# Kernel tuning notes

Hardware: AMD Instinct MI355X
Metric: run time of the kernel (lower is better)

Reference implementation:

```python
import jax, jax.numpy as jnp
import numpy as np

N = 50000      # nodes
E = 800000     # edges
IN = 128       # in_channels
H = 256        # hidden_channels
EMB = 128      # embedding_size
R = 4          # num_relations
HEADS = 2


def setup_inputs() -> dict:
    key = jax.random.key(0)
    ks = jax.random.split(key, 20)
    w = lambda k, shape: jax.random.normal(k, shape, dtype=jnp.float32) * 0.05
    return dict(
        x=jax.random.normal(ks[0], (N, IN), dtype=jnp.float32),
        edge_index=jax.random.randint(ks[1], (2, E), 0, N, dtype=jnp.int32),
        edge_type=jax.random.randint(ks[2], (E,), 0, R, dtype=jnp.int32),
        sage1_Wl=w(ks[3], (IN, H)), sage1_Wr=w(ks[4], (IN, H)), sage1_b=jnp.zeros((H,), jnp.float32),
        sage2_Wl=w(ks[5], (H, H)), sage2_Wr=w(ks[6], (H, H)), sage2_b=jnp.zeros((H,), jnp.float32),
        gat_W=w(ks[7], (H, HEADS * H)), gat_att_src=w(ks[8], (HEADS, H)), gat_att_dst=w(ks[9], (HEADS, H)),
        gat_b=jnp.zeros((H,), jnp.float32),
        rgcn_Wrel=w(ks[10], (R, H, EMB)), rgcn_Wroot=w(ks[11], (H, EMB)), rgcn_b=jnp.zeros((EMB,), jnp.float32),
        fusion_W=w(ks[12], (H + H + EMB, EMB)), fusion_b=jnp.zeros((EMB,), jnp.float32),
    )


def _segmean(msg, seg, num_segments):
    s = jax.ops.segment_sum(msg, seg, num_segments=num_segments)
    c = jax.ops.segment_sum(jnp.ones((seg.shape[0], 1), msg.dtype), seg, num_segments=num_segments)
    return s / jnp.maximum(c, 1.0)


def _sage(x, src, dst, Wl, Wr, b, n):
    # SAGEConv: lin_l(mean_j x_j) + lin_r(x_i)
    agg = _segmean(x[src], dst, n)
    return agg @ Wl + x @ Wr + b


def _gat(x, src, dst, W, a_src, a_dst, b, n):
    # GATConv heads=2, concat=False (head average), add_self_loops=True
    loop = jnp.arange(n, dtype=src.dtype)
    src = jnp.concatenate([src, loop])
    dst = jnp.concatenate([dst, loop])
    h = (x @ W).reshape(n, HEADS, -1)                 # [N, heads, H]
    al_src = (h * a_src).sum(-1)                      # [N, heads]
    al_dst = (h * a_dst).sum(-1)                      # [N, heads]
    e = jax.nn.leaky_relu(al_src[src] + al_dst[dst], 0.2)   # [E', heads]
    m = jax.ops.segment_max(e, dst, num_segments=n)          # stable softmax per dst node
    ex = jnp.exp(e - m[dst])
    den = jax.ops.segment_sum(ex, dst, num_segments=n)
    alpha = ex / jnp.maximum(den[dst], 1e-16)
    out = jax.ops.segment_sum(alpha[:, :, None] * h[src], dst, num_segments=n)  # [N, heads, H]
    return out.mean(axis=1) + b


def _rgcn(x, src, dst, etype, Wrel, Wroot, b, n, r):
    # RGCNConv: sum_r mean_{j in N_r(i)} W_r x_j + W_root x_i + b
    xt = jnp.einsum('nh,rhe->rne', x, Wrel)           # [R, N, EMB]
    m = xt[etype, src]                                # [E, EMB]
    seg = dst * r + etype                             # per (node, relation) segment
    agg = _segmean(m, seg, n * r).reshape(n, r, -1).sum(axis=1)
    return agg + x @ Wroot + b


def reference(x, edge_index, edge_type,
              sage1_Wl, sage1_Wr, sage1_b,
              sage2_Wl, sage2_Wr, sage2_b,
              gat_W, gat_att_src, gat_att_dst, gat_b,
              rgcn_Wrel, rgcn_Wroot, rgcn_b,
              fusion_W, fusion_b):
    src, dst = edge_index[0], edge_index[1]
    n = x.shape[0]
    x1 = jax.nn.relu(_sage(x, src, dst, sage1_Wl, sage1_Wr, sage1_b, n))
    # dropout(p=0.2) is identity in eval mode
    x_sage = jax.nn.relu(_sage(x1, src, dst, sage2_Wl, sage2_Wr, sage2_b, n))
    x_gat = jax.nn.relu(_gat(x_sage, src, dst, gat_W, gat_att_src, gat_att_dst, gat_b, n))
    x_rgcn = _rgcn(x_gat, src, dst, edge_type, rgcn_Wrel, rgcn_Wroot, rgcn_b, n, R)
    x_all = jnp.concatenate([x_sage, x_gat, x_rgcn], axis=1)
    out = x_all @ fusion_W + fusion_b
    norm = jnp.maximum(jnp.linalg.norm(out, axis=1, keepdims=True), 1e-12)
    return out / norm
```

## Files before the change

### kernel.cpp

```cpp
#include <hip/hip_runtime.h>
#include <math.h>

constexpr int NN   = 50000;
constexpr int NE   = 800000;
constexpr int NREL = 4;
constexpr int NB   = (NN + 255) / 256;

typedef __attribute__((ext_vector_type(8))) short bfrag;
typedef __attribute__((ext_vector_type(4))) float floatx4;

__device__ inline unsigned short bf16_rne(float x) {
  unsigned u = __float_as_uint(x);
  unsigned r = (u + 0x7FFFu + ((u >> 16) & 1u)) >> 16;
  return (unsigned short)r;
}
__device__ inline float bf2f(unsigned short h) {
  return __uint_as_float((unsigned)h << 16);
}
__device__ inline void split2(float x, unsigned short& h, unsigned short& l) {
  h = bf16_rne(x);
  l = bf16_rne(x - bf2f(h));
}

__global__ void k_counts(const int* __restrict__ src, const int* __restrict__ dst,
                         const int* __restrict__ et, int* deg, int* cntrel) {
  int e = blockIdx.x * blockDim.x + threadIdx.x;
  if (e < NE) {
    int d = dst[e];
    atomicAdd(&deg[d], 1);
    atomicAdd(&cntrel[d * NREL + et[e]], 1);
  }
}

__global__ void k_scan1(const int* __restrict__ deg, int* bsum) {
  __shared__ int sm[256];
  int i = blockIdx.x * 256 + threadIdx.x;
  sm[threadIdx.x] = (i < NN) ? deg[i] : 0;
  __syncthreads();
  for (int s = 128; s; s >>= 1) {
    if (threadIdx.x < s) sm[threadIdx.x] += sm[threadIdx.x + s];
    __syncthreads();
  }
  if (threadIdx.x == 0) bsum[blockIdx.x] = sm[0];
}
__global__ void k_scan2(const int* __restrict__ bsum, int* boff, int* rowptr) {
  if (threadIdx.x == 0 && blockIdx.x == 0) {
    int acc = 0;
    for (int b = 0; b < NB; ++b) { boff[b] = acc; acc += bsum[b]; }
    rowptr[NN] = NE;
  }
}
__global__ void k_scan3(const int* __restrict__ deg, const int* __restrict__ boff,
                        int* rowptr) {
  __shared__ int sm[256];
  int i = blockIdx.x * 256 + threadIdx.x;
  int v = (i < NN) ? deg[i] : 0;
  sm[threadIdx.x] = v;
  __syncthreads();
  for (int s = 1; s < 256; s <<= 1) {
    int t = (threadIdx.x >= s) ? sm[threadIdx.x - s] : 0;
    __syncthreads();
    sm[threadIdx.x] += t;
    __syncthreads();
  }
  if (i < NN) rowptr[i] = boff[blockIdx.x] + sm[threadIdx.x] - v;
}

__global__ void k_fill(const int* __restrict__ src, const int* __restrict__ dst,
                       const int* __restrict__ et, const int* __restrict__ rowptr,
                       int* cursor, int* srcs, int* ets) {
  int e = blockIdx.x * blockDim.x + threadIdx.x;
  if (e >= NE) return;
  int d = dst[e];
  int pos = rowptr[d] + atomicAdd(&cursor[d], 1);
  srcs[pos] = src[e];
  ets[pos]  = et[e];
}

#define PK_N 14
__device__ __constant__ const int PK_BASE[PK_N]  = {0,1,2,3,4,4,5,5,5,5,6,7,7,7};
__device__ __constant__ const int PK_EOFF[PK_N]  = {0,0,0,0,0,256,0,32768,65536,98304,0,0,32768,65536};
__device__ __constant__ const int PK_K[PK_N]     = {128,128,256,256,256,256,256,256,256,256,256,256,256,128};
__device__ __constant__ const int PK_LDB[PK_N]   = {256,256,256,256,512,512,128,128,128,128,128,128,128,128};
__device__ __constant__ const int PK_START[PK_N] = {0,4096,8192,16384,24576,32768,40960,45056,49152,53248,57344,61440,65536,69632};
constexpr int PK_TOTAL = 71680;
constexpr int BF_S1WL = 0,     BF_S1WR = 4096,  BF_S2WL = 8192,  BF_S2WR = 16384;
constexpr int BF_GATW0 = 24576, BF_GATW1 = 32768, BF_WREL = 40960, BF_WROOT = 57344;
constexpr int BF_FW0 = 61440,  BF_FW1 = 65536,  BF_FW2 = 69632;

__global__ void k_pack(const float* b0, const float* b1, const float* b2, const float* b3,
                       const float* b4, const float* b5, const float* b6, const float* b7,
                       unsigned short* __restrict__ Bh) {
  int f = blockIdx.x * 256 + threadIdx.x;
  if (f >= PK_TOTAL) return;
  int m = 0;
#pragma unroll
  for (int i = 1; i < PK_N; ++i) if (f >= PK_START[i]) m = i;
  const float* bases[8] = {b0,b1,b2,b3,b4,b5,b6,b7};
  int lf = f - PK_START[m];
  int K = PK_K[m], ldb = PK_LDB[m];
  int Kq16 = K << 1;
  int ntile = lf / Kq16;
  int rem = lf - ntile * Kq16;
  int kq = rem >> 4, c = rem & 15;
  const float* sp = bases[PK_BASE[m]] + PK_EOFF[m] + (size_t)(kq * 8) * ldb + ntile * 16 + c;
#pragma unroll
  for (int j = 0; j < 8; ++j)
    Bh[(size_t)f * 8 + j] = bf16_rne(sp[(size_t)j * ldb]);
}

__global__ void k_split(const float* __restrict__ x, unsigned short* __restrict__ xh,
                        unsigned short* __restrict__ xl, long total4) {
  long i = (long)blockIdx.x * blockDim.x + threadIdx.x;
  if (i >= total4) return;
  float4 v = ((const float4*)x)[i];
  ushort4 h, l;
  split2(v.x, h.x, l.x); split2(v.y, h.y, l.y);
  split2(v.z, h.z, l.z); split2(v.w, h.w, l.w);
  ((ushort4*)xh)[i] = h;
  ((ushort4*)xl)[i] = l;
}

__global__ void k_mean128p(const unsigned short* __restrict__ ih, const int* __restrict__ rowptr,
                           const int* __restrict__ srcs,
                           unsigned short* __restrict__ oh, unsigned short* __restrict__ ol) {
  int node = blockIdx.x * 4 + (threadIdx.x >> 6);
  int lane = threadIdx.x & 63;
  if (node >= NN) return;
  int p0 = rowptr[node], p1 = rowptr[node + 1];
  float2 acc = make_float2(0.f, 0.f);
  int p = p0;
  for (; p + 4 <= p1; p += 4) {
    int s0 = srcs[p], s1 = srcs[p+1], s2 = srcs[p+2], s3 = srcs[p+3];
    ushort2 v0 = ((const ushort2*)(ih + ((size_t)s0 << 7)))[lane];
    ushort2 v1 = ((const ushort2*)(ih + ((size_t)s1 << 7)))[lane];
    ushort2 v2 = ((const ushort2*)(ih + ((size_t)s2 << 7)))[lane];
    ushort2 v3 = ((const ushort2*)(ih + ((size_t)s3 << 7)))[lane];
    acc.x += (bf2f(v0.x) + bf2f(v1.x)) + (bf2f(v2.x) + bf2f(v3.x));
    acc.y += (bf2f(v0.y) + bf2f(v1.y)) + (bf2f(v2.y) + bf2f(v3.y));
  }
  for (; p < p1; ++p) {
    int s = srcs[p];
    ushort2 hv = ((const ushort2*)(ih + ((size_t)s << 7)))[lane];
    acc.x += bf2f(hv.x); acc.y += bf2f(hv.y);
  }
  float inv = (p1 > p0) ? 1.0f / (float)(p1 - p0) : 0.0f;
  ushort2 h, l;
  split2(acc.x * inv, h.x, l.x); split2(acc.y * inv, h.y, l.y);
  size_t o = ((size_t)node << 7) + lane * 2;
  *(ushort2*)(oh + o) = h;
  *(ushort2*)(ol + o) = l;
}

__global__ void k_mean256p(const unsigned short* __restrict__ ih, const int* __restrict__ rowptr,
                           const int* __restrict__ srcs,
                           unsigned short* __restrict__ oh, unsigned short* __restrict__ ol) {
  int node = blockIdx.x * 4 + (threadIdx.x >> 6);
  int lane = threadIdx.x & 63;
  if (node >= NN) return;
  int p0 = rowptr[node], p1 = rowptr[node + 1];
  float4 acc = make_float4(0.f, 0.f, 0.f, 0.f);
  int p = p0;
  for (; p + 8 <= p1; p += 8) {
    int ss[8]; ushort4 xr[8];
#pragma unroll
    for (int j = 0; j < 8; ++j) ss[j] = srcs[p + j];
#pragma unroll
    for (int j = 0; j < 8; ++j)
      xr[j] = *(const ushort4*)(ih + ((size_t)ss[j] << 8) + lane * 4);
#pragma unroll
    for (int j = 0; j < 8; ++j) {
      acc.x += bf2f(xr[j].x); acc.y += bf2f(xr[j].y);
      acc.z += bf2f(xr[j].z); acc.w += bf2f(xr[j].w);
    }
  }
  for (; p < p1; ++p) {
    int s = srcs[p];
    ushort4 hv = *(const ushort4*)(ih + ((size_t)s << 8) + lane * 4);
    acc.x += bf2f(hv.x); acc.y += bf2f(hv.y);
    acc.z += bf2f(hv.z); acc.w += bf2f(hv.w);
  }
  float inv = (p1 > p0) ? 1.0f / (float)(p1 - p0) : 0.0f;
  ushort4 h, l;
  split2(acc.x * inv, h.x, l.x); split2(acc.y * inv, h.y, l.y);
  split2(acc.z * inv, h.z, l.z); split2(acc.w * inv, h.w, l.w);
  size_t o = ((size_t)node << 8) + lane * 4;
  *(ushort4*)(oh + o) = h;
  *(ushort4*)(ol + o) = l;
}

__global__ __launch_bounds__(256)
void k_gemm_mfma(const unsigned short* __restrict__ Bph,
                 const unsigned short* A0h, const unsigned short* A0l, int lda0, int bf0, int K0,
                 const unsigned short* A1h, const unsigned short* A1l, int lda1, int bf1, int K1,
                 const unsigned short* A2h, const unsigned short* A2l, int lda2, int bf2, int K2,
                 const float* __restrict__ bias, float* Cf,
                 unsigned short* Ch, unsigned short* Cl,
                 int M, int Nc, float scale, int do_relu, int zsB, long zsC, int xtmode)
{
  __shared__ short Ash[8*64*8], Asl[8*64*8], Bsh[8*64*8];
  const int tid  = threadIdx.x;
  const int lane = tid & 63;
  const int wv   = tid >> 6;
  const int wm   = wv >> 1, wn = wv & 1;
  const int nwg = gridDim.x * gridDim.y;
  const int d   = blockIdx.x + gridDim.x * blockIdx.y;
  const int q   = nwg >> 3, r = nwg & 7;
  const int xcd = d & 7, di = d >> 3;
  const int wg  = (xcd < r ? xcd * (q + 1) : r * (q + 1) + (xcd - r) * q) + di;
  const int row0 = (wg / gridDim.x) * 128;
  const int col0 = (wg % gridDim.x) * 128;
  if (zsB) {
    bf0 += blockIdx.z * zsB;
    long zc = (long)blockIdx.z * zsC;
    if (Cf) Cf += zc;
    if (Ch) { Ch += zc; if (Cl) Cl += zc; }
  }

  floatx4 acc[4][4];
#pragma unroll
  for (int i = 0; i < 4; ++i)
#pragma unroll
    for (int j = 0; j < 4; ++j) acc[i][j] = 0;

  const int a_m = tid >> 1;
  const int a_h = tid & 1;
  const int b_nt = tid >> 5;
  const int b_rem = (tid << 1) & 63;

  const unsigned short* Aharr[3] = {A0h, A1h, A2h};
  const unsigned short* Alarr[3] = {A0l, A1l, A2l};
  const int ldaArr[3] = {lda0, lda1, lda2};
  const int bfArr[3]  = {bf0, bf1, bf2};
  const int Karr[3]   = {K0, K1, K2};

  for (int p = 0; p < 3; ++p) {
    const int K = Karr[p];
    if (K == 0) continue;
    const int lda = ldaArr[p];
    const bool arow_ok = (row0 + a_m) < M;
    const unsigned short* Arh = Aharr[p] + (size_t)(row0 + a_m) * lda + a_h * 16;
    const unsigned short* Arl = Alarr[p] + (size_t)(row0 + a_m) * lda + a_h * 16;
    const int Kq16 = K << 1;
    const int bbase = bfArr[p] + (col0 >> 4) * Kq16 + b_nt * Kq16 + b_rem;

    for (int kt = 0; kt < K; kt += 32) {
      bfrag ah0, ah1, al0, al1;
      if (arow_ok) {
        ah0 = *(const bfrag*)(Arh + kt);
        ah1 = *(const bfrag*)(Arh + kt + 8);
        al0 = *(const bfrag*)(Arl + kt);
        al1 = *(const bfrag*)(Arl + kt + 8);
      } else {
#pragma unroll
        for (int i = 0; i < 8; ++i) { ah0[i]=0; ah1[i]=0; al0[i]=0; al1[i]=0; }
      }
      const unsigned short* bp_h = Bph + (size_t)(bbase + (kt << 1)) * 8;
      bfrag bh0 = *(const bfrag*)bp_h;
      bfrag bh1 = *(const bfrag*)(bp_h + 8);

      __syncthreads();
      {
        int q2 = a_h * 2;
        int i0 = ((a_m >> 4) * 64 + ((a_m & 15) | (q2 << 4))) * 8;
        int i1 = ((a_m >> 4) * 64 + ((a_m & 15) | ((q2 + 1) << 4))) * 8;
        *(bfrag*)&Ash[i0] = ah0;  *(bfrag*)&Ash[i1] = ah1;
        *(bfrag*)&Asl[i0] = al0;  *(bfrag*)&Asl[i1] = al1;
      }
      {
        int f0 = tid * 2;
        *(bfrag*)&Bsh[(size_t)f0 * 8] = bh0;
        *(bfrag*)&Bsh[(size_t)(f0 + 1) * 8] = bh1;
      }
      __syncthreads();

      bfrag afh[4], afl[4], bfh[4];
#pragma unroll
      for (int mt = 0; mt < 4; ++mt) {
        int idx = ((wm * 4 + mt) * 64 + lane) * 8;
        afh[mt] = *(bfrag*)&Ash[idx];
        afl[mt] = *(bfrag*)&Asl[idx];
      }
#pragma unroll
      for (int nt = 0; nt < 4; ++nt) {
        int idx = ((wn * 4 + nt) * 64 + lane) * 8;
        bfh[nt] = *(bfrag*)&Bsh[idx];
      }
#pragma unroll
      for (int mt = 0; mt < 4; ++mt)
#pragma unroll
        for (int nt = 0; nt < 4; ++nt) {
          acc[mt][nt] = __builtin_amdgcn_mfma_f32_16x16x32_bf16(afh[mt], bfh[nt], acc[mt][nt], 0, 0, 0);
          acc[mt][nt] = __builtin_amdgcn_mfma_f32_16x16x32_bf16(afl[mt], bfh[nt], acc[mt][nt], 0, 0, 0);
        }
    }
  }

  const int cl = lane & 15;
  const int rq = lane >> 4;
#pragma unroll
  for (int mt = 0; mt < 4; ++mt)
#pragma unroll
    for (int r2 = 0; r2 < 4; ++r2) {
      int row = row0 + wm * 64 + mt * 16 + rq * 4 + r2;
      if (row < M) {
#pragma unroll
        for (int nt = 0; nt < 4; ++nt) {
          int colx = col0 + wn * 64 + nt * 16 + cl;
          float vraw = acc[mt][nt][r2] * scale;
          if (xtmode == 2) {
            if (colx < 512) {
              size_t o = (size_t)(colx >> 7) * ((size_t)NN * 128) + (size_t)row * 128 + (colx & 127);
              Ch[o] = bf16_rne(vraw);
            } else {
              size_t o = (size_t)row * 128 + (colx & 127);
              Cf[o] = vraw + (bias ? bias[colx & 127] : 0.0f);
            }
          } else {
            float v = vraw + (bias ? bias[colx] : 0.0f);
            if (do_relu) v = fmaxf(v, 0.0f);
            size_t o = (size_t)row * Nc + colx;
            if (Cf) Cf[o] = v;
            if (Ch) {
              if (Cl) {
                unsigned short h, l; split2(v, h, l);
                Ch[o] = h; Cl[o] = l;
              } else {
                Ch[o] = bf16_rne(v);
              }
            }
          }
        }
      }
    }
}

__global__ void k_wtilde(const float* __restrict__ gatW, const float* __restrict__ att_s,
                         const float* __restrict__ att_d, float* __restrict__ wt) {
  int k = threadIdx.x;
  const float* Wr = gatW + (size_t)k * 512;
  float s0 = 0, s1 = 0, d0 = 0, d1 = 0;
  for (int i = 0; i < 256; ++i) {
    float w0 = Wr[i], w1 = Wr[256 + i];
    s0 += w0 * att_s[i];       s1 += w1 * att_s[256 + i];
    d0 += w0 * att_d[i];       d1 += w1 * att_d[256 + i];
  }
  wt[k] = s0; wt[256 + k] = s1; wt[512 + k] = d0; wt[768 + k] = d1;
}

__global__ void k_al(const unsigned short* __restrict__ xsh_, const float* __restrict__ wt,
                     float* __restrict__ al_s, float* __restrict__ al_d) {
  int node = blockIdx.x * 4 + (threadIdx.x >> 6);
  int lane = threadIdx.x & 63;
  if (node >= NN) return;
  ushort4 hv = *(const ushort4*)(xsh_ + (size_t)node * 256 + lane * 4);
  float4 v = make_float4(bf2f(hv.x), bf2f(hv.y), bf2f(hv.z), bf2f(hv.w));
  const float4* w = (const float4*)wt;
  float4 a0 = w[lane], a1 = w[64 + lane], a2 = w[128 + lane], a3 = w[192 + lane];
  float s0 = v.x*a0.x + v.y*a0.y + v.z*a0.z + v.w*a0.w;
  float s1 = v.x*a1.x + v.y*a1.y + v.z*a1.z + v.w*a1.w;
  float s2 = v.x*a2.x + v.y*a2.y + v.z*a2.z + v.w*a2.w;
  float s3 = v.x*a3.x + v.y*a3.y + v.z*a3.z + v.w*a3.w;
  for (int off = 32; off; off >>= 1) {
    s0 += __shfl_down(s0, off); s1 += __shfl_down(s1, off);
    s2 += __shfl_down(s2, off); s3 += __shfl_down(s3, off);
  }
  if (lane == 0) {
    al_s[node*2] = s0; al_s[node*2 + 1] = s1;
    al_d[node*2] = s2; al_d[node*2 + 1] = s3;
  }
}

__device__ inline float lrelu(float v) { return v > 0.f ? v : 0.2f * v; }

__global__ void k_gat_csr(const unsigned short* __restrict__ xsh_,
                          const int* __restrict__ rowptr, const int* __restrict__ srcs,
                          const float* __restrict__ als, const float* __restrict__ ald,
                          float2* __restrict__ es,
                          unsigned short* __restrict__ aggh, unsigned short* __restrict__ aggl) {
  int node = blockIdx.x * 4 + (threadIdx.x >> 6);
  int lane = threadIdx.x & 63;
  if (node >= NN) return;
  int p0 = rowptr[node], p1 = rowptr[node + 1];
  float bd0 = ald[node*2], bd1 = ald[node*2 + 1];
  float vs0 = lrelu(als[node*2] + bd0);
  float vs1 = lrelu(als[node*2 + 1] + bd1);

  float t0 = 0.f, t1 = 0.f;
  for (int p = p0 + lane; p < p1; p += 64) {
    int s = srcs[p];
    float2 a = *(const float2*)(als + (size_t)s * 2);
    float e0 = __expf(lrelu(a.x + bd0));
    float e1 = __expf(lrelu(a.y + bd1));
    es[p] = make_float2(e0, e1);
    t0 += e0; t1 += e1;
  }
  for (int off = 32; off; off >>= 1) {
    t0 += __shfl_xor(t0, off);
    t1 += __shfl_xor(t1, off);
  }
  float w0 = __expf(vs0), w1 = __expf(vs1);
  float den0 = t0 + w0, den1 = t1 + w1;
  __threadfence_block();

  ushort4 hv = *(const ushort4*)(xsh_ + (size_t)node * 256 + lane * 4);
  float4 v = make_float4(bf2f(hv.x), bf2f(hv.y), bf2f(hv.z), bf2f(hv.w));
  float4 acc0 = make_float4(w0*v.x, w0*v.y, w0*v.z, w0*v.w);
  float4 acc1 = make_float4(w1*v.x, w1*v.y, w1*v.z, w1*v.w);
  int p = p0;
  for (; p + 8 <= p1; p += 8) {
    int ss[8]; float2 ee[8]; ushort4 xr[8];
#pragma unroll
    for (int j = 0; j < 8; ++j) ss[j] = srcs[p + j];
#pragma unroll
    for (int j = 0; j < 8; ++j) ee[j] = es[p + j];
#pragma unroll
    for (int j = 0; j < 8; ++j)
      xr[j] = *(const ushort4*)(xsh_ + (size_t)ss[j] * 256 + lane * 4);
#pragma unroll
    for (int j = 0; j < 8; ++j) {
      float4 xv = make_float4(bf2f(xr[j].x), bf2f(xr[j].y), bf2f(xr[j].z), bf2f(xr[j].w));
      acc0.x += ee[j].x*xv.x; acc0.y += ee[j].x*xv.y;
      acc0.z += ee[j].x*xv.z; acc0.w += ee[j].x*xv.w;
      acc1.x += ee[j].y*xv.x; acc1.y += ee[j].y*xv.y;
      acc1.z += ee[j].y*xv.z; acc1.w += ee[j].y*xv.w;
    }
  }
  for (; p < p1; ++p) {
    int s = srcs[p];
    float2 e = es[p];
    ushort4 xh4 = *(const ushort4*)(xsh_ + (size_t)s * 256 + lane * 4);
    float4 xv = make_float4(bf2f(xh4.x), bf2f(xh4.y), bf2f(xh4.z), bf2f(xh4.w));
    acc0.x += e.x*xv.x; acc0.y += e.x*xv.y; acc0.z += e.x*xv.z; acc0.w += e.x*xv.w;
    acc1.x += e.y*xv.x; acc1.y += e.y*xv.y; acc1.z += e.y*xv.z; acc1.w += e.y*xv.w;
  }
  float i0 = 1.0f / fmaxf(den0, 1e-16f);
  float i1 = 1.0f / fmaxf(den1, 1e-16f);
  ushort4 h, l;
  size_t o = (size_t)node * 512 + lane * 4;
  split2(acc0.x*i0, h.x, l.x); split2(acc0.y*i0, h.y, l.y);
  split2(acc0.z*i0, h.z, l.z); split2(acc0.w*i0, h.w, l.w);
  *(ushort4*)(aggh + o) = h; *(ushort4*)(aggl + o) = l;
  split2(acc1.x*i1, h.x, l.x); split2(acc1.y*i1, h.y, l.y);
  split2(acc1.z*i1, h.z, l.z); split2(acc1.w*i1, h.w, l.w);
  *(ushort4*)(aggh + o + 256) = h; *(ushort4*)(aggl + o + 256) = l;
}

__global__ void k_rgcn_csr(const unsigned short* __restrict__ xth,
                           const int* __restrict__ rowptr, const int* __restrict__ srcs,
                           const int* __restrict__ ets, const int* __restrict__ cntrel,
                           const float* __restrict__ P3f,
                           unsigned short* __restrict__ oh, unsigned short* __restrict__ ol) {
  int node = blockIdx.x * 4 + (threadIdx.x >> 6);
  int lane = threadIdx.x & 63;
  if (node >= NN) return;
  int p0 = rowptr[node], p1 = rowptr[node + 1];
  float inv0, inv1, inv2, inv3;
  {
    int c0 = cntrel[node*NREL], c1 = cntrel[node*NREL+1];
    int c2 = cntrel[node*NREL+2], c3 = cntrel[node*NREL+3];
    inv0 = c0 ? 1.0f/(float)c0 : 0.0f;  inv1 = c1 ? 1.0f/(float)c1 : 0.0f;
    inv2 = c2 ? 1.0f/(float)c2 : 0.0f;  inv3 = c3 ? 1.0f/(float)c3 : 0.0f;
  }
  float2 acc = ((const float2*)(P3f + ((size_t)node << 7)))[lane];
  int p = p0;
  for (; p + 8 <= p1; p += 8) {
    int ss[8], rr[8]; ushort2 xr[8];
#pragma unroll
    for (int j = 0; j < 8; ++j) { ss[j] = srcs[p + j]; rr[j] = ets[p + j]; }
#pragma unroll
    for (int j = 0; j < 8; ++j)
      xr[j] = *(const ushort2*)(xth + (((size_t)rr[j] * NN + ss[j]) << 7) + lane * 2);
#pragma unroll
    for (int j = 0; j < 8; ++j) {
      float w = (rr[j] == 0) ? inv0 : (rr[j] == 1) ? inv1 : (rr[j] == 2) ? inv2 : inv3;
      acc.x += bf2f(xr[j].x) * w;
      acc.y += bf2f(xr[j].y) * w;
    }
  }
  for (; p < p1; ++p) {
    int s = srcs[p], r = ets[p];
    ushort2 hv = *(const ushort2*)(xth + (((size_t)r * NN + s) << 7) + lane * 2);
    float w = (r == 0) ? inv0 : (r == 1) ? inv1 : (r == 2) ? inv2 : inv3;
    acc.x += bf2f(hv.x) * w;
    acc.y += bf2f(hv.y) * w;
  }
  ushort2 h, l;
  split2(acc.x, h.x, l.x); split2(acc.y, h.y, l.y);
  size_t o = ((size_t)node << 7) + lane * 2;
  *(ushort2*)(oh + o) = h;
  *(ushort2*)(ol + o) = l;
}

__global__ void k_norm(float* __restrict__ out) {
  int gw = (int)(((long)blockIdx.x * blockDim.x + threadIdx.x) >> 6);
  int lane = threadIdx.x & 63;
  if (gw >= NN) return;
  float2* row = (float2*)(out + (size_t)gw * 128);
  float2 v = row[lane];
  float ss = v.x*v.x + v.y*v.y;
  for (int off = 32; off; off >>= 1) ss += __shfl_down(ss, off);
  ss = __shfl(ss, 0);
  float inv = 1.0f / fmaxf(sqrtf(ss), 1e-12f);
  row[lane] = make_float2(v.x*inv, v.y*inv);
}

extern "C" void kernel_launch(void* const* d_in, const int* in_sizes, int n_in,
                              void* d_out, int out_size, void* d_ws, size_t ws_size,
                              hipStream_t stream)
{
  const float* x     = (const float*)d_in[0];
  const int*   ei    = (const int*)d_in[1];
  const int*   etype = (const int*)d_in[2];
  const float* s1Wl  = (const float*)d_in[3];
  const float* s1Wr  = (const float*)d_in[4];
  const float* s1b   = (const float*)d_in[5];
  const float* s2Wl  = (const float*)d_in[6];
  const float* s2Wr  = (const float*)d_in[7];
  const float* s2b   = (const float*)d_in[8];
  const float* gatW  = (const float*)d_in[9];
  const float* att_s = (const float*)d_in[10];
  const float* att_d = (const float*)d_in[11];
  const float* gatb  = (const float*)d_in[12];
  const float* Wrel  = (const float*)d_in[13];
  const float* Wroot = (const float*)d_in[14];
  const float* rgcnb = (const float*)d_in[15];
  const float* fW    = (const float*)d_in[16];
  const float* fb    = (const float*)d_in[17];
  float* out = (float*)d_out;

  const int* src = ei;
  const int* dst = ei + NE;

  char* ws = (char*)d_ws;
  size_t off = 0;
  auto alloc = [&](size_t bytes) -> void* {
    void* p = ws + off;
    off = (off + bytes + 255) & ~(size_t)255;
    return p;
  };
  int*      deg    = (int*)alloc((size_t)NN * 4);
  int*      cntrel = (int*)alloc((size_t)NN * NREL * 4);
  int*      rowptr = (int*)alloc((size_t)(NN + 1) * 4);
  int*      cursor = (int*)alloc((size_t)NN * 4);
  int*      bsum   = (int*)alloc((size_t)NB * 4);
  int*      boff   = (int*)alloc((size_t)NB * 4);
  int*      srcs   = (int*)alloc((size_t)NE * 4);
  int*      ets    = (int*)alloc((size_t)NE * 4);
  float*    al_s   = (float*)alloc((size_t)NN * 2 * 4);
  float*    al_d   = (float*)alloc((size_t)NN * 2 * 4);
  float*    wt     = (float*)alloc((size_t)4 * 256 * 4);
  unsigned short* PBh = (unsigned short*)alloc((size_t)PK_TOTAL * 8 * 2);
  char* SAb = (char*)alloc((size_t)NN * 1024);
  char* SBb = (char*)alloc((size_t)NN * 1024);
  char* SCb = (char*)alloc((size_t)NN * 1024);
  char* SDb = (char*)alloc((size_t)NN * 1024);
  (void)ws_size; (void)in_sizes; (void)n_in; (void)out_size;

  unsigned short* xh  = (unsigned short*)SAb;
  unsigned short* xl  = xh + (size_t)NN * 128;
  unsigned short* m1h = xl + (size_t)NN * 128;
  unsigned short* m1l = m1h + (size_t)NN * 128;
  unsigned short* aggh = (unsigned short*)SAb;
  float*          P3f  = (float*)SAb;
  unsigned short* p3h  = (unsigned short*)(SAb + (size_t)NN * 512);
  unsigned short* p3l  = p3h + (size_t)NN * 128;
  unsigned short* x1h = (unsigned short*)SBb;
  unsigned short* x1l = x1h + (size_t)NN * 256;
  unsigned short* aggl = (unsigned short*)SBb;
  unsigned short* xth = (unsigned short*)SBb;
  unsigned short* m2h = (unsigned short*)SCb;
  unsigned short* m2l = m2h + (size_t)NN * 256;
  float2*         es  = (float2*)SCb;
  unsigned short* xgh = (unsigned short*)SCb;
  unsigned short* xgl = xgh + (size_t)NN * 256;
  unsigned short* xsh = (unsigned short*)SDb;
  unsigned short* xsl = xsh + (size_t)NN * 256;

  const int NODEB = (NN + 3) / 4;
  const int GY = (NN + 127) / 128;

  k_pack<<<(PK_TOTAL + 255) / 256, 256, 0, stream>>>(s1Wl, s1Wr, s2Wl, s2Wr, gatW, Wrel, Wroot, fW, PBh);
  hipMemsetAsync(deg, 0, (size_t)NN * 4, stream);
  hipMemsetAsync(cntrel, 0, (size_t)NN * NREL * 4, stream);
  hipMemsetAsync(cursor, 0, (size_t)NN * 4, stream);
  k_counts<<<(NE + 255) / 256, 256, 0, stream>>>(src, dst, etype, deg, cntrel);
  k_scan1<<<NB, 256, 0, stream>>>(deg, bsum);
  k_scan2<<<1, 64, 0, stream>>>(bsum, boff, rowptr);
  k_scan3<<<NB, 256, 0, stream>>>(deg, boff, rowptr);
  k_fill<<<(NE + 255) / 256, 256, 0, stream>>>(src, dst, etype, rowptr, cursor, srcs, ets);
  k_split<<<((NN * 128 / 4) + 255) / 256, 256, 0, stream>>>(x, xh, xl, (long)NN * 128 / 4);

  k_mean128p<<<NODEB, 256, 0, stream>>>(xh, rowptr, srcs, m1h, m1l);
  k_gemm_mfma<<<dim3(2, GY, 1), 256, 0, stream>>>(PBh,
      m1h, m1l, 128, BF_S1WL, 128,  xh, xl, 128, BF_S1WR, 128,  nullptr, nullptr, 0, 0, 0,
      s1b, nullptr, x1h, x1l, NN, 256, 1.0f, 1, 0, 0, 0);

  k_mean256p<<<NODEB, 256, 0, stream>>>(x1h, rowptr, srcs, m2h, m2l);
  k_gemm_mfma<<<dim3(2, GY, 1), 256, 0, stream>>>(PBh,
      m2h, m2l, 256, BF_S2WL, 256,  x1h, x1l, 256, BF_S2WR, 256,  nullptr, nullptr, 0, 0, 0,
      s2b, nullptr, xsh, xsl, NN, 256, 1.0f, 1, 0, 0, 0);

  k_wtilde<<<1, 256, 0, stream>>>(gatW, att_s, att_d, wt);
  k_al<<<NODEB, 256, 0, stream>>>(xsh, wt, al_s, al_d);
  k_gat_csr<<<NODEB, 256, 0, stream>>>(xsh, rowptr, srcs, al_s, al_d, es, aggh, aggl);
  k_gemm_mfma<<<dim3(2, GY, 1), 256, 0, stream>>>(PBh,
      aggh, aggl, 512, BF_GATW0, 256,  aggh + 256, aggl + 256, 512, BF_GATW1, 256,
      nullptr, nullptr, 0, 0, 0,
      gatb, nullptr, xgh, xgl, NN, 256, 0.5f, 1, 0, 0, 0);

  k_gemm_mfma<<<dim3(5, GY, 1), 256, 0, stream>>>(PBh,
      xgh, xgl, 256, BF_WREL, 256,  nullptr, nullptr, 0, 0, 0,  nullptr, nullptr, 0, 0, 0,
      rgcnb, P3f, xth, nullptr, NN, 640, 1.0f, 0, 0, 0, 2);
  k_rgcn_csr<<<NODEB, 256, 0, stream>>>(xth, rowptr, srcs, ets, cntrel, P3f, p3h, p3l);

  k_gemm_mfma<<<dim3(1, GY, 1), 256, 0, stream>>>(PBh,
      xsh, xsl, 256, BF_FW0, 256,  xgh, xgl, 256, BF_FW1, 256,  p3h, p3l, 128, BF_FW2, 128,
      fb, out, nullptr, nullptr, NN, 128, 1.0f, 0, 0, 0, 0);
  k_norm<<<(NN + 3) / 4, 256, 0, stream>>>(out);
}
```

Baseline: 830.5 us.

## Split each node's gather across two wavefronts and derive degree from relation counts

All four CSR gather kernels (two mean kernels, the GAT aggregation and the RGCN aggregation) now give each destination node two wavefronts instead of one. The wavefronts interleave 8-edge chunks and combine their partial sums through shared memory. This doubles the memory-level parallelism per node for the latency-bound neighbour gathers, at the cost of a block barrier, extra LDS traffic and half the lanes idling in the epilogue. Separately, the per-node degree atomic is removed: degree is recomputed by summing the four relation counts with an int4 load. This drops one atomic per edge and one memset.

```diff
diff --git a/kernel.cpp b/kernel.cpp
--- a/kernel.cpp
+++ b/kernel.cpp
@@ -22,20 +22,21 @@
   l = bf16_rne(x - bf2f(h));
 }
 
-__global__ void k_counts(const int* __restrict__ src, const int* __restrict__ dst,
-                         const int* __restrict__ et, int* deg, int* cntrel) {
+__global__ void k_counts(const int* __restrict__ dst, const int* __restrict__ et,
+                         int* cntrel) {
   int e = blockIdx.x * blockDim.x + threadIdx.x;
   if (e < NE) {
     int d = dst[e];
-    atomicAdd(&deg[d], 1);
     atomicAdd(&cntrel[d * NREL + et[e]], 1);
   }
 }
 
-__global__ void k_scan1(const int* __restrict__ deg, int* bsum) {
+__global__ void k_scan1(const int* __restrict__ cntrel, int* bsum) {
   __shared__ int sm[256];
   int i = blockIdx.x * 256 + threadIdx.x;
-  sm[threadIdx.x] = (i < NN) ? deg[i] : 0;
+  int v = 0;
+  if (i < NN) { int4 c = ((const int4*)cntrel)[i]; v = c.x + c.y + c.z + c.w; }
+  sm[threadIdx.x] = v;
   __syncthreads();
   for (int s = 128; s; s >>= 1) {
     if (threadIdx.x < s) sm[threadIdx.x] += sm[threadIdx.x + s];
@@ -50,11 +51,12 @@
     rowptr[NN] = NE;
   }
 }
-__global__ void k_scan3(const int* __restrict__ deg, const int* __restrict__ boff,
+__global__ void k_scan3(const int* __restrict__ cntrel, const int* __restrict__ boff,
                         int* rowptr) {
   __shared__ int sm[256];
   int i = blockIdx.x * 256 + threadIdx.x;
-  int v = (i < NN) ? deg[i] : 0;
+  int v = 0;
+  if (i < NN) { int4 c = ((const int4*)cntrel)[i]; v = c.x + c.y + c.z + c.w; }
   sm[threadIdx.x] = v;
   __syncthreads();
   for (int s = 1; s < 256; s <<= 1) {
@@ -124,44 +126,60 @@
 __global__ void k_mean128p(const unsigned short* __restrict__ ih, const int* __restrict__ rowptr,
                            const int* __restrict__ srcs,
                            unsigned short* __restrict__ oh, unsigned short* __restrict__ ol) {
-  int node = blockIdx.x * 4 + (threadIdx.x >> 6);
+  __shared__ float comb[2][2][64];
+  int pair = threadIdx.x >> 7;
+  int w    = (threadIdx.x >> 6) & 1;
   int lane = threadIdx.x & 63;
-  if (node >= NN) return;
+  int node = blockIdx.x * 2 + pair;
   int p0 = rowptr[node], p1 = rowptr[node + 1];
+  int deg = p1 - p0;
+  int nfull = deg >> 3;
   float2 acc = make_float2(0.f, 0.f);
-  int p = p0;
-  for (; p + 4 <= p1; p += 4) {
-    int s0 = srcs[p], s1 = srcs[p+1], s2 = srcs[p+2], s3 = srcs[p+3];
-    ushort2 v0 = ((const ushort2*)(ih + ((size_t)s0 << 7)))[lane];
-    ushort2 v1 = ((const ushort2*)(ih + ((size_t)s1 << 7)))[lane];
-    ushort2 v2 = ((const ushort2*)(ih + ((size_t)s2 << 7)))[lane];
-    ushort2 v3 = ((const ushort2*)(ih + ((size_t)s3 << 7)))[lane];
-    acc.x += (bf2f(v0.x) + bf2f(v1.x)) + (bf2f(v2.x) + bf2f(v3.x));
-    acc.y += (bf2f(v0.y) + bf2f(v1.y)) + (bf2f(v2.y) + bf2f(v3.y));
-  }
-  for (; p < p1; ++p) {
-    int s = srcs[p];
-    ushort2 hv = ((const ushort2*)(ih + ((size_t)s << 7)))[lane];
-    acc.x += bf2f(hv.x); acc.y += bf2f(hv.y);
-  }
-  float inv = (p1 > p0) ? 1.0f / (float)(p1 - p0) : 0.0f;
-  ushort2 h, l;
-  split2(acc.x * inv, h.x, l.x); split2(acc.y * inv, h.y, l.y);
-  size_t o = ((size_t)node << 7) + lane * 2;
-  *(ushort2*)(oh + o) = h;
-  *(ushort2*)(ol + o) = l;
+  for (int c = w; c < nfull; c += 2) {
+    int p = p0 + c * 8;
+    int ss[8]; ushort2 xr[8];
+#pragma unroll
+    for (int j = 0; j < 8; ++j) ss[j] = srcs[p + j];
+#pragma unroll
+    for (int j = 0; j < 8; ++j)
+      xr[j] = ((const ushort2*)(ih + ((size_t)ss[j] << 7)))[lane];
+#pragma unroll
+    for (int j = 0; j < 8; ++j) { acc.x += bf2f(xr[j].x); acc.y += bf2f(xr[j].y); }
+  }
+  if (w == 0) {
+    for (int p = p0 + nfull * 8; p < p1; ++p) {
+      int s = srcs[p];
+      ushort2 hv = ((const ushort2*)(ih + ((size_t)s << 7)))[lane];
+      acc.x += bf2f(hv.x); acc.y += bf2f(hv.y);
+    }
+  }
+  if (w == 1) { comb[pair][0][lane] = acc.x; comb[pair][1][lane] = acc.y; }
+  __syncthreads();
+  if (w == 0) {
+    acc.x += comb[pair][0][lane]; acc.y += comb[pair][1][lane];
+    float inv = deg ? 1.0f / (float)deg : 0.0f;
+    ushort2 h, l;
+    split2(acc.x * inv, h.x, l.x); split2(acc.y * inv, h.y, l.y);
+    size_t o = ((size_t)node << 7) + lane * 2;
+    *(ushort2*)(oh + o) = h;
+    *(ushort2*)(ol + o) = l;
+  }
 }
 
 __global__ void k_mean256p(const unsigned short* __restrict__ ih, const int* __restrict__ rowptr,
                            const int* __restrict__ srcs,
                            unsigned short* __restrict__ oh, unsigned short* __restrict__ ol) {
-  int node = blockIdx.x * 4 + (threadIdx.x >> 6);
+  __shared__ float comb[2][4][64];
+  int pair = threadIdx.x >> 7;
+  int w    = (threadIdx.x >> 6) & 1;
   int lane = threadIdx.x & 63;
-  if (node >= NN) return;
+  int node = blockIdx.x * 2 + pair;
   int p0 = rowptr[node], p1 = rowptr[node + 1];
+  int deg = p1 - p0;
+  int nfull = deg >> 3;
   float4 acc = make_float4(0.f, 0.f, 0.f, 0.f);
-  int p = p0;
-  for (; p + 8 <= p1; p += 8) {
+  for (int c = w; c < nfull; c += 2) {
+    int p = p0 + c * 8;
     int ss[8]; ushort4 xr[8];
 #pragma unroll
     for (int j = 0; j < 8; ++j) ss[j] = srcs[p + j];
@@ -174,19 +192,30 @@
       acc.z += bf2f(xr[j].z); acc.w += bf2f(xr[j].w);
     }
   }
-  for (; p < p1; ++p) {
-    int s = srcs[p];
-    ushort4 hv = *(const ushort4*)(ih + ((size_t)s << 8) + lane * 4);
-    acc.x += bf2f(hv.x); acc.y += bf2f(hv.y);
-    acc.z += bf2f(hv.z); acc.w += bf2f(hv.w);
-  }
-  float inv = (p1 > p0) ? 1.0f / (float)(p1 - p0) : 0.0f;
-  ushort4 h, l;
-  split2(acc.x * inv, h.x, l.x); split2(acc.y * inv, h.y, l.y);
-  split2(acc.z * inv, h.z, l.z); split2(acc.w * inv, h.w, l.w);
-  size_t o = ((size_t)node << 8) + lane * 4;
-  *(ushort4*)(oh + o) = h;
-  *(ushort4*)(ol + o) = l;
+  if (w == 0) {
+    for (int p = p0 + nfull * 8; p < p1; ++p) {
+      int s = srcs[p];
+      ushort4 hv = *(const ushort4*)(ih + ((size_t)s << 8) + lane * 4);
+      acc.x += bf2f(hv.x); acc.y += bf2f(hv.y);
+      acc.z += bf2f(hv.z); acc.w += bf2f(hv.w);
+    }
+  }
+  if (w == 1) {
+    comb[pair][0][lane] = acc.x; comb[pair][1][lane] = acc.y;
+    comb[pair][2][lane] = acc.z; comb[pair][3][lane] = acc.w;
+  }
+  __syncthreads();
+  if (w == 0) {
+    acc.x += comb[pair][0][lane]; acc.y += comb[pair][1][lane];
+    acc.z += comb[pair][2][lane]; acc.w += comb[pair][3][lane];
+    float inv = deg ? 1.0f / (float)deg : 0.0f;
+    ushort4 h, l;
+    split2(acc.x * inv, h.x, l.x); split2(acc.y * inv, h.y, l.y);
+    split2(acc.z * inv, h.z, l.z); split2(acc.w * inv, h.w, l.w);
+    size_t o = ((size_t)node << 8) + lane * 4;
+    *(ushort4*)(oh + o) = h;
+    *(ushort4*)(ol + o) = l;
+  }
 }
 
 __global__ __launch_bounds__(256)
@@ -378,16 +407,20 @@
                           const float* __restrict__ als, const float* __restrict__ ald,
                           float2* __restrict__ es,
                           unsigned short* __restrict__ aggh, unsigned short* __restrict__ aggl) {
-  int node = blockIdx.x * 4 + (threadIdx.x >> 6);
+  __shared__ float comb[2][8][64];
+  __shared__ float denl[2][2];
+  int pair = threadIdx.x >> 7;
+  int w    = (threadIdx.x >> 6) & 1;
   int lane = threadIdx.x & 63;
-  if (node >= NN) return;
+  int node = blockIdx.x * 2 + pair;
   int p0 = rowptr[node], p1 = rowptr[node + 1];
+  int deg = p1 - p0;
   float bd0 = ald[node*2], bd1 = ald[node*2 + 1];
   float vs0 = lrelu(als[node*2] + bd0);
   float vs1 = lrelu(als[node*2 + 1] + bd1);
 
   float t0 = 0.f, t1 = 0.f;
-  for (int p = p0 + lane; p < p1; p += 64) {
+  for (int p = p0 + w * 64 + lane; p < p1; p += 128) {
     int s = srcs[p];
     float2 a = *(const float2*)(als + (size_t)s * 2);
     float e0 = __expf(lrelu(a.x + bd0));
@@ -399,16 +432,21 @@
     t0 += __shfl_xor(t0, off);
     t1 += __shfl_xor(t1, off);
   }
+  if (w == 1 && lane == 0) { denl[pair][0] = t0; denl[pair][1] = t1; }
+  __syncthreads();
+
+  float4 acc0 = make_float4(0.f, 0.f, 0.f, 0.f);
+  float4 acc1 = make_float4(0.f, 0.f, 0.f, 0.f);
   float w0 = __expf(vs0), w1 = __expf(vs1);
-  float den0 = t0 + w0, den1 = t1 + w1;
-  __threadfence_block();
-
-  ushort4 hv = *(const ushort4*)(xsh_ + (size_t)node * 256 + lane * 4);
-  float4 v = make_float4(bf2f(hv.x), bf2f(hv.y), bf2f(hv.z), bf2f(hv.w));
-  float4 acc0 = make_float4(w0*v.x, w0*v.y, w0*v.z, w0*v.w);
-  float4 acc1 = make_float4(w1*v.x, w1*v.y, w1*v.z, w1*v.w);
-  int p = p0;
-  for (; p + 8 <= p1; p += 8) {
+  if (w == 0) {
+    ushort4 hv = *(const ushort4*)(xsh_ + (size_t)node * 256 + lane * 4);
+    float4 v = make_float4(bf2f(hv.x), bf2f(hv.y), bf2f(hv.z), bf2f(hv.w));
+    acc0 = make_float4(w0*v.x, w0*v.y, w0*v.z, w0*v.w);
+    acc1 = make_float4(w1*v.x, w1*v.y, w1*v.z, w1*v.w);
+  }
+  int nfull = deg >> 3;
+  for (int c = w; c < nfull; c += 2) {
+    int p = p0 + c * 8;
     int ss[8]; float2 ee[8]; ushort4 xr[8];
 #pragma unroll
     for (int j = 0; j < 8; ++j) ss[j] = srcs[p + j];
@@ -426,24 +464,41 @@
       acc1.z += ee[j].y*xv.z; acc1.w += ee[j].y*xv.w;
     }
   }
-  for (; p < p1; ++p) {
-    int s = srcs[p];
-    float2 e = es[p];
-    ushort4 xh4 = *(const ushort4*)(xsh_ + (size_t)s * 256 + lane * 4);
-    float4 xv = make_float4(bf2f(xh4.x), bf2f(xh4.y), bf2f(xh4.z), bf2f(xh4.w));
-    acc0.x += e.x*xv.x; acc0.y += e.x*xv.y; acc0.z += e.x*xv.z; acc0.w += e.x*xv.w;
-    acc1.x += e.y*xv.x; acc1.y += e.y*xv.y; acc1.z += e.y*xv.z; acc1.w += e.y*xv.w;
-  }
-  float i0 = 1.0f / fmaxf(den0, 1e-16f);
-  float i1 = 1.0f / fmaxf(den1, 1e-16f);
-  ushort4 h, l;
-  size_t o = (size_t)node * 512 + lane * 4;
-  split2(acc0.x*i0, h.x, l.x); split2(acc0.y*i0, h.y, l.y);
-  split2(acc0.z*i0, h.z, l.z); split2(acc0.w*i0, h.w, l.w);
-  *(ushort4*)(aggh + o) = h; *(ushort4*)(aggl + o) = l;
-  split2(acc1.x*i1, h.x, l.x); split2(acc1.y*i1, h.y, l.y);
-  split2(acc1.z*i1, h.z, l.z); split2(acc1.w*i1, h.w, l.w);
-  *(ushort4*)(aggh + o + 256) = h; *(ushort4*)(aggl + o + 256) = l;
+  if (w == 0) {
+    for (int p = p0 + nfull * 8; p < p1; ++p) {
+      int s = srcs[p];
+      float2 e = es[p];
+      ushort4 xh4 = *(const ushort4*)(xsh_ + (size_t)s * 256 + lane * 4);
+      float4 xv = make_float4(bf2f(xh4.x), bf2f(xh4.y), bf2f(xh4.z), bf2f(xh4.w));
+      acc0.x += e.x*xv.x; acc0.y += e.x*xv.y; acc0.z += e.x*xv.z; acc0.w += e.x*xv.w;
+      acc1.x += e.y*xv.x; acc1.y += e.y*xv.y; acc1.z += e.y*xv.z; acc1.w += e.y*xv.w;
+    }
+  }
+  if (w == 1) {
+    comb[pair][0][lane] = acc0.x; comb[pair][1][lane] = acc0.y;
+    comb[pair][2][lane] = acc0.z; comb[pair][3][lane] = acc0.w;
+    comb[pair][4][lane] = acc1.x; comb[pair][5][lane] = acc1.y;
+    comb[pair][6][lane] = acc1.z; comb[pair][7][lane] = acc1.w;
+  }
+  __syncthreads();
+  if (w == 0) {
+    acc0.x += comb[pair][0][lane]; acc0.y += comb[pair][1][lane];
+    acc0.z += comb[pair][2][lane]; acc0.w += comb[pair][3][lane];
+    acc1.x += comb[pair][4][lane]; acc1.y += comb[pair][5][lane];
+    acc1.z += comb[pair][6][lane]; acc1.w += comb[pair][7][lane];
+    float den0 = t0 + denl[pair][0] + w0;
+    float den1 = t1 + denl[pair][1] + w1;
+    float i0 = 1.0f / fmaxf(den0, 1e-16f);
+    float i1 = 1.0f / fmaxf(den1, 1e-16f);
+    ushort4 h, l;
+    size_t o = (size_t)node * 512 + lane * 4;
+    split2(acc0.x*i0, h.x, l.x); split2(acc0.y*i0, h.y, l.y);
+    split2(acc0.z*i0, h.z, l.z); split2(acc0.w*i0, h.w, l.w);
+    *(ushort4*)(aggh + o) = h; *(ushort4*)(aggl + o) = l;
+    split2(acc1.x*i1, h.x, l.x); split2(acc1.y*i1, h.y, l.y);
+    split2(acc1.z*i1, h.z, l.z); split2(acc1.w*i1, h.w, l.w);
+    *(ushort4*)(aggh + o + 256) = h; *(ushort4*)(aggl + o + 256) = l;
+  }
 }
 
 __global__ void k_rgcn_csr(const unsigned short* __restrict__ xth,
@@ -451,20 +506,24 @@
                            const int* __restrict__ ets, const int* __restrict__ cntrel,
                            const float* __restrict__ P3f,
                            unsigned short* __restrict__ oh, unsigned short* __restrict__ ol) {
-  int node = blockIdx.x * 4 + (threadIdx.x >> 6);
+  __shared__ float comb[2][2][64];
+  int pair = threadIdx.x >> 7;
+  int w    = (threadIdx.x >> 6) & 1;
   int lane = threadIdx.x & 63;
-  if (node >= NN) return;
+  int node = blockIdx.x * 2 + pair;
   int p0 = rowptr[node], p1 = rowptr[node + 1];
+  int deg = p1 - p0;
   float inv0, inv1, inv2, inv3;
   {
-    int c0 = cntrel[node*NREL], c1 = cntrel[node*NREL+1];
-    int c2 = cntrel[node*NREL+2], c3 = cntrel[node*NREL+3];
-    inv0 = c0 ? 1.0f/(float)c0 : 0.0f;  inv1 = c1 ? 1.0f/(float)c1 : 0.0f;
-    inv2 = c2 ? 1.0f/(float)c2 : 0.0f;  inv3 = c3 ? 1.0f/(float)c3 : 0.0f;
-  }
-  float2 acc = ((const float2*)(P3f + ((size_t)node << 7)))[lane];
-  int p = p0;
-  for (; p + 8 <= p1; p += 8) {
+    int4 c = ((const int4*)cntrel)[node];
+    inv0 = c.x ? 1.0f/(float)c.x : 0.0f;  inv1 = c.y ? 1.0f/(float)c.y : 0.0f;
+    inv2 = c.z ? 1.0f/(float)c.z : 0.0f;  inv3 = c.w ? 1.0f/(float)c.w : 0.0f;
+  }
+  float2 acc = make_float2(0.f, 0.f);
+  if (w == 0) acc = ((const float2*)(P3f + ((size_t)node << 7)))[lane];
+  int nfull = deg >> 3;
+  for (int c = w; c < nfull; c += 2) {
+    int p = p0 + c * 8;
     int ss[8], rr[8]; ushort2 xr[8];
 #pragma unroll
     for (int j = 0; j < 8; ++j) { ss[j] = srcs[p + j]; rr[j] = ets[p + j]; }
@@ -473,23 +532,30 @@
       xr[j] = *(const ushort2*)(xth + (((size_t)rr[j] * NN + ss[j]) << 7) + lane * 2);
 #pragma unroll
     for (int j = 0; j < 8; ++j) {
-      float w = (rr[j] == 0) ? inv0 : (rr[j] == 1) ? inv1 : (rr[j] == 2) ? inv2 : inv3;
-      acc.x += bf2f(xr[j].x) * w;
-      acc.y += bf2f(xr[j].y) * w;
-    }
-  }
-  for (; p < p1; ++p) {
-    int s = srcs[p], r = ets[p];
-    ushort2 hv = *(const ushort2*)(xth + (((size_t)r * NN + s) << 7) + lane * 2);
-    float w = (r == 0) ? inv0 : (r == 1) ? inv1 : (r == 2) ? inv2 : inv3;
-    acc.x += bf2f(hv.x) * w;
-    acc.y += bf2f(hv.y) * w;
-  }
-  ushort2 h, l;
-  split2(acc.x, h.x, l.x); split2(acc.y, h.y, l.y);
-  size_t o = ((size_t)node << 7) + lane * 2;
-  *(ushort2*)(oh + o) = h;
-  *(ushort2*)(ol + o) = l;
+      float wgt = (rr[j] == 0) ? inv0 : (rr[j] == 1) ? inv1 : (rr[j] == 2) ? inv2 : inv3;
+      acc.x += bf2f(xr[j].x) * wgt;
+      acc.y += bf2f(xr[j].y) * wgt;
+    }
+  }
+  if (w == 0) {
+    for (int p = p0 + nfull * 8; p < p1; ++p) {
+      int s = srcs[p], r = ets[p];
+      ushort2 hv = *(const ushort2*)(xth + (((size_t)r * NN + s) << 7) + lane * 2);
+      float wgt = (r == 0) ? inv0 : (r == 1) ? inv1 : (r == 2) ? inv2 : inv3;
+      acc.x += bf2f(hv.x) * wgt;
+      acc.y += bf2f(hv.y) * wgt;
+    }
+  }
+  if (w == 1) { comb[pair][0][lane] = acc.x; comb[pair][1][lane] = acc.y; }
+  __syncthreads();
+  if (w == 0) {
+    acc.x += comb[pair][0][lane]; acc.y += comb[pair][1][lane];
+    ushort2 h, l;
+    split2(acc.x, h.x, l.x); split2(acc.y, h.y, l.y);
+    size_t o = ((size_t)node << 7) + lane * 2;
+    *(ushort2*)(oh + o) = h;
+    *(ushort2*)(ol + o) = l;
+  }
 }
 
 __global__ void k_norm(float* __restrict__ out) {
@@ -555,7 +621,7 @@
   char* SBb = (char*)alloc((size_t)NN * 1024);
   char* SCb = (char*)alloc((size_t)NN * 1024);
   char* SDb = (char*)alloc((size_t)NN * 1024);
-  (void)ws_size; (void)in_sizes; (void)n_in; (void)out_size;
+  (void)deg; (void)ws_size; (void)in_sizes; (void)n_in; (void)out_size;
 
   unsigned short* xh  = (unsigned short*)SAb;
   unsigned short* xl  = xh + (size_t)NN * 128;
@@ -577,33 +643,33 @@
   unsigned short* xsh = (unsigned short*)SDb;
   unsigned short* xsl = xsh + (size_t)NN * 256;
 
-  const int NODEB = (NN + 3) / 4;
+  const int NODEB  = (NN + 3) / 4;
+  const int NODEB2 = NN / 2;
   const int GY = (NN + 127) / 128;
 
   k_pack<<<(PK_TOTAL + 255) / 256, 256, 0, stream>>>(s1Wl, s1Wr, s2Wl, s2Wr, gatW, Wrel, Wroot, fW, PBh);
-  hipMemsetAsync(deg, 0, (size_t)NN * 4, stream);
   hipMemsetAsync(cntrel, 0, (size_t)NN * NREL * 4, stream);
   hipMemsetAsync(cursor, 0, (size_t)NN * 4, stream);
-  k_counts<<<(NE + 255) / 256, 256, 0, stream>>>(src, dst, etype, deg, cntrel);
-  k_scan1<<<NB, 256, 0, stream>>>(deg, bsum);
+  k_counts<<<(NE + 255) / 256, 256, 0, stream>>>(dst, etype, cntrel);
+  k_scan1<<<NB, 256, 0, stream>>>(cntrel, bsum);
   k_scan2<<<1, 64, 0, stream>>>(bsum, boff, rowptr);
-  k_scan3<<<NB, 256, 0, stream>>>(deg, boff, rowptr);
+  k_scan3<<<NB, 256, 0, stream>>>(cntrel, boff, rowptr);
   k_fill<<<(NE + 255) / 256, 256, 0, stream>>>(src, dst, etype, rowptr, cursor, srcs, ets);
   k_split<<<((NN * 128 / 4) + 255) / 256, 256, 0, stream>>>(x, xh, xl, (long)NN * 128 / 4);
 
-  k_mean128p<<<NODEB, 256, 0, stream>>>(xh, rowptr, srcs, m1h, m1l);
+  k_mean128p<<<NODEB2, 256, 0, stream>>>(xh, rowptr, srcs, m1h, m1l);
   k_gemm_mfma<<<dim3(2, GY, 1), 256, 0, stream>>>(PBh,
       m1h, m1l, 128, BF_S1WL, 128,  xh, xl, 128, BF_S1WR, 128,  nullptr, nullptr, 0, 0, 0,
       s1b, nullptr, x1h, x1l, NN, 256, 1.0f, 1, 0, 0, 0);
 
-  k_mean256p<<<NODEB, 256, 0, stream>>>(x1h, rowptr, srcs, m2h, m2l);
+  k_mean256p<<<NODEB2, 256, 0, stream>>>(x1h, rowptr, srcs, m2h, m2l);
   k_gemm_mfma<<<dim3(2, GY, 1), 256, 0, stream>>>(PBh,
       m2h, m2l, 256, BF_S2WL, 256,  x1h, x1l, 256, BF_S2WR, 256,  nullptr, nullptr, 0, 0, 0,
       s2b, nullptr, xsh, xsl, NN, 256, 1.0f, 1, 0, 0, 0);
 
   k_wtilde<<<1, 256, 0, stream>>>(gatW, att_s, att_d, wt);
   k_al<<<NODEB, 256, 0, stream>>>(xsh, wt, al_s, al_d);
-  k_gat_csr<<<NODEB, 256, 0, stream>>>(xsh, rowptr, srcs, al_s, al_d, es, aggh, aggl);
+  k_gat_csr<<<NODEB2, 256, 0, stream>>>(xsh, rowptr, srcs, al_s, al_d, es, aggh, aggl);
   k_gemm_mfma<<<dim3(2, GY, 1), 256, 0, stream>>>(PBh,
       aggh, aggl, 512, BF_GATW0, 256,  aggh + 256, aggl + 256, 512, BF_GATW1, 256,
       nullptr, nullptr, 0, 0, 0,
@@ -612,7 +678,7 @@
   k_gemm_mfma<<<dim3(5, GY, 1), 256, 0, stream>>>(PBh,
       xgh, xgl, 256, BF_WREL, 256,  nullptr, nullptr, 0, 0, 0,  nullptr, nullptr, 0, 0, 0,
       rgcnb, P3f, xth, nullptr, NN, 640, 1.0f, 0, 0, 0, 2);
-  k_rgcn_csr<<<NODEB, 256, 0, stream>>>(xth, rowptr, srcs, ets, cntrel, P3f, p3h, p3l);
+  k_rgcn_csr<<<NODEB2, 256, 0, stream>>>(xth, rowptr, srcs, ets, cntrel, P3f, p3h, p3l);
 
   k_gemm_mfma<<<dim3(1, GY, 1), 256, 0, stream>>>(PBh,
       xsh, xsl, 256, BF_FW0, 256,  xgh, xgl, 256, BF_FW1, 256,  p3h, p3l, 128, BF_FW2, 128,
```

After: 890.1 us. +7.2%, slower.
